# Kernel optimization log

Hardware: AMD Instinct MI355X
Metric: run time of the kernel (lower is better)

## Reference

```python
import jax, jax.numpy as jnp
import numpy as np

TAU = 3.0          # CPG tau
VTH = 1.0          # LIF v_threshold (v_reset = 0, hard reset)
PEAK = 16          # peak population size
NUM_E = 25         # int(32 * 0.8) excitatory neurons
FATIGUE_TH = 8
ALPHA = 4.0        # spikingjelly sigmoid surrogate alpha (unused in fwd)


def spike_fn(x):
    # Heaviside threshold at 0 (v >= VTH fires)
    return (x >= 0.0).astype(x.dtype)


def setup_inputs() -> dict:
    key = jax.random.key(0)
    k0, k1, k2, k3, k4 = jax.random.split(key, 5)
    B, N = 524288, 32
    spike_history = (jax.random.uniform(k0, (B, N)) < 0.3).astype(jnp.float32)
    neighbor_E_spikes = (jax.random.uniform(k1, (B, 8, NUM_E)) < 0.3).astype(jnp.float32)
    # mutual_inhibition: -2.0 everywhere, within-population blocks *0.1 -> -0.2,
    # cross-population blocks set to -3.0
    is_peak = jnp.arange(N) < PEAK
    same_pop = is_peak[:, None] == is_peak[None, :]
    mutual_inhibition = jnp.where(same_pop, -0.2, -3.0).astype(jnp.float32)
    coupling_W = jax.random.normal(k2, (N, NUM_E), dtype=jnp.float32) * 0.2
    peak_fatigue = jax.random.randint(k3, (B,), 0, 10, dtype=jnp.int32)
    trough_fatigue = jax.random.randint(k4, (B,), 0, 10, dtype=jnp.int32)
    v0 = jnp.zeros((B, N), dtype=jnp.float32)
    return {
        "spike_history": spike_history,
        "neighbor_E_spikes": neighbor_E_spikes,
        "mutual_inhibition": mutual_inhibition,
        "coupling_W": coupling_W,
        "v0": v0,
        "peak_fatigue": peak_fatigue,
        "trough_fatigue": trough_fatigue,
        "num_ticks": 5,
    }


def reference(spike_history, neighbor_E_spikes, mutual_inhibition, coupling_W,
              v0, peak_fatigue, trough_fatigue, num_ticks):
    B = spike_history.shape[0]
    # fatigue-driven drive: trough fatigue excites peak half, peak fatigue excites trough half
    dp = jnp.where(trough_fatigue >= FATIGUE_TH, 2.0, 0.0)[:, None]  # [B,1]
    dt = jnp.where(peak_fatigue >= FATIGUE_TH, 2.0, 0.0)[:, None]
    drive = jnp.concatenate(
        [jnp.broadcast_to(dp, (B, PEAK)), jnp.broadcast_to(dt, (B, 32 - PEAK))], axis=-1)
    # neighbor coupling: sum_k W @ nbr_k ; constant across ticks, hoisted out of loop
    coupling = jnp.einsum('bkn,mn->bm', neighbor_E_spikes, coupling_W)
    base = drive + 0.3 * coupling  # [B,32]

    def step(carry, _):
        v, sh, acc = carry
        recurrent = jnp.einsum('bn,mn->bm', sh, mutual_inhibition)  # sh @ M.T
        x = base + 0.5 * recurrent
        # LIF (decay_input=True): v += (x - (v - v_reset)) / tau, v_reset = 0
        v = v + (x - v) / TAU
        s = spike_fn(v - VTH)
        v = v * (1.0 - s)  # hard reset to 0
        return (v, s, acc + s), None

    init = (v0, spike_history, jnp.zeros_like(v0))
    (v, sh, acc), _ = jax.lax.scan(step, init, None, length=num_ticks)
    should_stay = acc[:, PEAK:].sum(axis=-1) > 0.5  # trough active => STAY
    return acc[:, :NUM_E], should_stay
```

## Files before the change

kernel.cpp:

```cpp
#include <hip/hip_runtime.h>


#define FATIGUE_TH 8

__device__ __forceinline__ void async_f4(const float* g, float* l) {
    __builtin_amdgcn_global_load_lds(
        (const __attribute__((address_space(1))) void*)g,
        (__attribute__((address_space(3))) void*)l, 16, 0, 0);
}

__global__ __launch_bounds__(256, 4) void AgentLSM_70841190580507_kernel(
    const float* __restrict__ sh_in,
    const float* __restrict__ nbr,
    const float* __restrict__ M,
    const float* __restrict__ W,
    const int*   __restrict__ pf,
    const int*   __restrict__ tf,
    const int*   __restrict__ ticks_p,
    float* __restrict__ out_acc,
    float* __restrict__ out_stay,
    int B, int nchunks, int cpb)
{
    __shared__ float lds_nbr[2][1600];
    __shared__ float lds_cnt[8 * 28];

    const int tid = threadIdx.x;
    const int g   = tid >> 5;
    const int m   = tid & 31;
    const bool is_peak = (m < 16);

    if (tid < 200) async_f4(W + tid * 4, &lds_nbr[0][tid * 4]);
    __syncthreads();
    float w[28];
    #pragma unroll
    for (int n = 0; n < 25; ++n) w[n] = lds_nbr[0][m * 25 + n];
    w[25] = 0.f; w[26] = 0.f; w[27] = 0.f;
    const float a_same  = M[0];
    const float a_cross = M[16];
    const int T = ticks_p[0];
    __syncthreads();

    const int first = blockIdx.x * cpb;
    if (first >= nchunks) return;
    const int count = min(cpb, nchunks - first);

    #define STAGE(c, buf) do {                                                \
        const float* _src = nbr + (long long)(c) * 1600;                      \
        float* _dst = lds_nbr[(buf)];                                         \
        if ((long long)((c) + 1) * 8 <= (long long)B) {                       \
            async_f4(_src + tid * 4, _dst + tid * 4);                         \
            if (tid < 144) async_f4(_src + (tid + 256) * 4,                   \
                                    _dst + (tid + 256) * 4);                  \
        } else {                 \
            const long long _ftot = (long long)B * 200 - (long long)(c) * 1600;\
            for (int _i = tid; _i < 400; _i += 256) {                         \
                float4 _v = make_float4(0.f, 0.f, 0.f, 0.f);                  \
                if ((long long)_i * 4 + 3 < _ftot)                            \
                    _v = ((const float4*)_src)[_i];                           \
                ((float4*)_dst)[_i] = _v;                                     \
            }                                                                 \
        }                                                                     \
    } while (0)

    STAGE(first, 0);
    __syncthreads();

    int cur = 0;
    for (int j = 0; j < count; ++j) {
        const int c = first + j;
        const long long b = (long long)c * 8 + g;
        const bool valid = (b < (long long)B);

        float drive = 0.f;
        int init_bit = 0;
        if (valid) {
            drive = is_peak ? ((tf[b] >= FATIGUE_TH) ? 2.0f : 0.0f)
                            : ((pf[b] >= FATIGUE_TH) ? 2.0f : 0.0f);
            init_bit = (sh_in[b * 32 + m] != 0.0f);
        }

        if (m < 28) {
            float cv = 0.f;
            if (m < 25) {
                #pragma unroll
                for (int k = 0; k < 8; ++k) cv += lds_nbr[cur][g * 200 + k * 25 + m];
            }
            lds_cnt[g * 28 + m] = cv;
        }
        __syncthreads();

        if (j + 1 < count) STAGE(c + 1, cur ^ 1);

        float coup = 0.f;
        {
            const float4* c4p = (const float4*)&lds_cnt[g * 28];
            #pragma unroll
            for (int q = 0; q < 7; ++q) {
                float4 c4 = c4p[q];
                coup += c4.x * w[4*q+0] + c4.y * w[4*q+1]
                      + c4.z * w[4*q+2] + c4.w * w[4*q+3];
            }
        }

        const float base = drive + 0.3f * coup;
        float v = 0.0f;

        unsigned long long bal = __ballot(init_bit);
        unsigned int mask = (unsigned int)(bal >> (tid & 32));

        int acc = 0;
        unsigned int any_tr = 0;

        #define TICK()  do {                                                   \
            float Spf = (float)__popc(mask & 0xFFFFu);                         \
            float Stf = (float)__popc(mask >> 16);                             \
            float rec = is_peak ? (a_same * Spf + a_cross * Stf)               \
                                : (a_cross * Spf + a_same * Stf);              \
            float x = base + 0.5f * rec;                                       \
            v = v + (x - v) / 3.0f;                  \
            bool s = (v >= 1.0f);                 \
            unsigned long long sb = __ballot(s);                               \
            mask = (unsigned int)(sb >> (tid & 32));                           \
            any_tr |= (mask >> 16);                                            \
            acc += s ? 1 : 0;                                                  \
            v = s ? 0.0f : v;                                                  \
        } while (0)

        if (T == 5) {
            TICK(); TICK(); TICK(); TICK(); TICK();
        } else {
            for (int t = 0; t < T; ++t) TICK();
        }
        #undef TICK

        if (valid) {
            if (m < 25) out_acc[(long long)c * 200 + g * 25 + m] = (float)acc;
            if (m == 0) out_stay[b] = any_tr ? 1.0f : 0.0f;
        }

        __syncthreads();
        cur ^= 1;
    }
    #undef STAGE
}

extern "C" void kernel_launch(void* const* d_in, const int* in_sizes, int n_in,
                              void* d_out, int out_size, void* d_ws, size_t ws_size,
                              hipStream_t stream) {
    const float* sh    = (const float*)d_in[0];
    const float* nbr   = (const float*)d_in[1];
    const float* M     = (const float*)d_in[2];
    const float* W     = (const float*)d_in[3];
    const int*   pf    = (const int*)d_in[5];
    const int*   tf    = (const int*)d_in[6];
    const int*   ticks = (const int*)d_in[7];

    const int B = in_sizes[5];
    float* out_acc  = (float*)d_out;
    float* out_stay = out_acc + (long long)B * 25;

    const int nchunks = (B + 7) / 8;
    int grid = nchunks < 8192 ? nchunks : 8192;
    int cpb  = (nchunks + grid - 1) / grid;
    grid = (nchunks + cpb - 1) / cpb;
    AgentLSM_70841190580507_kernel<<<grid, 256, 0, stream>>>(
        sh, nbr, M, W, pf, tf, ticks, out_acc, out_stay, B, nchunks, cpb);
}
```

Before: 636.9 us.

## Drop LDS double-buffered staging; load neighbor spikes directly per lane

Removes the async global-to-LDS double-buffered staging of neighbor spikes and the block-wide barriers. Each lane now reads its eight neighbor values straight from global memory and reduces them in registers. Only the small per-group count vector goes through LDS, fenced with a waitcnt instead of __syncthreads, since each 32-lane group reads back only its own slots. It also halves the grid cap and drops the occupancy hint in launch bounds. The cost is less latency hiding for the strided global loads.

```diff
diff --git a/kernel.cpp b/kernel.cpp
--- a/kernel.cpp
+++ b/kernel.cpp
@@ -3,13 +3,7 @@
 
 #define FATIGUE_TH 8
 
-__device__ __forceinline__ void async_f4(const float* g, float* l) {
-    __builtin_amdgcn_global_load_lds(
-        (const __attribute__((address_space(1))) void*)g,
-        (__attribute__((address_space(3))) void*)l, 16, 0, 0);
-}
-
-__global__ __launch_bounds__(256, 4) void AgentLSM_70841190580507_kernel(
+__global__ __launch_bounds__(256) void AgentLSM_70841190580507_kernel(
     const float* __restrict__ sh_in,
     const float* __restrict__ nbr,
     const float* __restrict__ M,
@@ -21,56 +15,36 @@
     float* __restrict__ out_stay,
     int B, int nchunks, int cpb)
 {
-    __shared__ float lds_nbr[2][1600];
-    __shared__ float lds_cnt[8 * 28];
+    __shared__ float4 lds_cnt4[8][7];
 
     const int tid = threadIdx.x;
     const int g   = tid >> 5;
     const int m   = tid & 31;
     const bool is_peak = (m < 16);
 
-    if (tid < 200) async_f4(W + tid * 4, &lds_nbr[0][tid * 4]);
-    __syncthreads();
     float w[28];
     #pragma unroll
-    for (int n = 0; n < 25; ++n) w[n] = lds_nbr[0][m * 25 + n];
+    for (int n = 0; n < 25; ++n) w[n] = W[m * 25 + n];
     w[25] = 0.f; w[26] = 0.f; w[27] = 0.f;
+
     const float a_same  = M[0];
     const float a_cross = M[16];
     const int T = ticks_p[0];
-    __syncthreads();
 
     const int first = blockIdx.x * cpb;
-    if (first >= nchunks) return;
-    const int count = min(cpb, nchunks - first);
+    const int lastc = min(first + cpb, nchunks);
 
-    #define STAGE(c, buf) do {                                                \
-        const float* _src = nbr + (long long)(c) * 1600;                      \
-        float* _dst = lds_nbr[(buf)];                                         \
-        if ((long long)((c) + 1) * 8 <= (long long)B) {                       \
-            async_f4(_src + tid * 4, _dst + tid * 4);                         \
-            if (tid < 144) async_f4(_src + (tid + 256) * 4,                   \
-                                    _dst + (tid + 256) * 4);                  \
-        } else {                 \
-            const long long _ftot = (long long)B * 200 - (long long)(c) * 1600;\
-            for (int _i = tid; _i < 400; _i += 256) {                         \
-                float4 _v = make_float4(0.f, 0.f, 0.f, 0.f);                  \
-                if ((long long)_i * 4 + 3 < _ftot)                            \
-                    _v = ((const float4*)_src)[_i];                           \
-                ((float4*)_dst)[_i] = _v;                                     \
-            }                                                                 \
-        }                                                                     \
-    } while (0)
-
-    STAGE(first, 0);
-    __syncthreads();
-
-    int cur = 0;
-    for (int j = 0; j < count; ++j) {
-        const int c = first + j;
+    for (int c = first; c < lastc; ++c) {
         const long long b = (long long)c * 8 + g;
         const bool valid = (b < (long long)B);
 
+        float cv = 0.f;
+        if (valid && m < 25) {
+            const float* p = nbr + b * 200 + m;
+            float x0 = p[0],   x1 = p[25],  x2 = p[50],  x3 = p[75];
+            float x4 = p[100], x5 = p[125], x6 = p[150], x7 = p[175];
+            cv = ((x0 + x1) + (x2 + x3)) + ((x4 + x5) + (x6 + x7));
+        }
         float drive = 0.f;
         int init_bit = 0;
         if (valid) {
@@ -79,27 +53,16 @@
             init_bit = (sh_in[b * 32 + m] != 0.0f);
         }
 
-        if (m < 28) {
-            float cv = 0.f;
-            if (m < 25) {
-                #pragma unroll
-                for (int k = 0; k < 8; ++k) cv += lds_nbr[cur][g * 200 + k * 25 + m];
-            }
-            lds_cnt[g * 28 + m] = cv;
-        }
-        __syncthreads();
-
-        if (j + 1 < count) STAGE(c + 1, cur ^ 1);
+        if (m < 28) ((float*)&lds_cnt4[g][0])[m] = (m < 25) ? cv : 0.f;
+        asm volatile("s_waitcnt lgkmcnt(0)" ::: "memory");
+        __builtin_amdgcn_sched_barrier(0);
 
         float coup = 0.f;
-        {
-            const float4* c4p = (const float4*)&lds_cnt[g * 28];
-            #pragma unroll
-            for (int q = 0; q < 7; ++q) {
-                float4 c4 = c4p[q];
-                coup += c4.x * w[4*q+0] + c4.y * w[4*q+1]
-                      + c4.z * w[4*q+2] + c4.w * w[4*q+3];
-            }
+        #pragma unroll
+        for (int q = 0; q < 7; ++q) {
+            float4 c4 = lds_cnt4[g][q];
+            coup += c4.x * w[4*q+0] + c4.y * w[4*q+1]
+                  + c4.z * w[4*q+2] + c4.w * w[4*q+3];
         }
 
         const float base = drive + 0.3f * coup;
@@ -137,11 +100,7 @@
             if (m < 25) out_acc[(long long)c * 200 + g * 25 + m] = (float)acc;
             if (m == 0) out_stay[b] = any_tr ? 1.0f : 0.0f;
         }
-
-        __syncthreads();
-        cur ^= 1;
     }
-    #undef STAGE
 }
 
 extern "C" void kernel_launch(void* const* d_in, const int* in_sizes, int n_in,
@@ -160,7 +119,7 @@
     float* out_stay = out_acc + (long long)B * 25;
 
     const int nchunks = (B + 7) / 8;
-    int grid = nchunks < 8192 ? nchunks : 8192;
+    int grid = nchunks < 4096 ? nchunks : 4096;
     int cpb  = (nchunks + grid - 1) / grid;
     grid = (nchunks + cpb - 1) / cpb;
     AgentLSM_70841190580507_kernel<<<grid, 256, 0, stream>>>(
```

New measurement: 645.4 us. No clear change (+1.3%).
